# Kernel optimization log

Measured on AMD Instinct MI355X. Metric: run time of the kernel, lower is better.

## Reference

```python
import jax, jax.numpy as jnp
import numpy as np

B, C, H, W = 4, 3, 512, 960
K2 = 16  # 4x4 adaptive filter, DAIN-style


def setup_inputs() -> dict:
    key = jax.random.key(0)
    k1, k2, k3 = jax.random.split(key, 3)
    teninput = jax.random.normal(k1, (B, C, H, W), dtype=jnp.float32)
    tenflow = jax.random.normal(k2, (B, 2, H, W), dtype=jnp.float32)
    tenfilter = jax.random.uniform(k3, (B, K2, H, W), dtype=jnp.float32)
    return {"teninput": teninput, "tenflow": tenflow, "tenfilter": tenfilter}


def reference(teninput, tenflow, tenfilter):
    # DAIN FilterInterpolation forward:
    # out[b,c,y,x] = valid * sum_{dj,di < K} filter[b, dj*K+di, y, x]
    #               * bilinear(input, y2_T + dj + beta, x2_L + di + alpha)
    # with per-corner clamped gathers; out-of-bounds flow targets give 0.
    b, c, h, w = teninput.shape
    k2 = tenfilter.shape[1]
    K = int(np.sqrt(k2))

    dt = teninput.dtype
    xs = jnp.arange(w, dtype=dt)[None, None, :]
    ys = jnp.arange(h, dtype=dt)[None, :, None]
    fx, fy = tenflow[:, 0], tenflow[:, 1]          # [B,H,W]
    x2 = xs + fx
    y2 = ys + fy
    valid = ((x2 >= 0) & (x2 <= w - 1) & (y2 >= 0) & (y2 <= h - 1)
             & (jnp.abs(fx) < w / 2) & (jnp.abs(fy) < h / 2))

    ix = jnp.floor(x2).astype(jnp.int32)
    iy = jnp.floor(y2).astype(jnp.int32)
    alpha = (x2 - ix)[:, None]                     # [B,1,H,W]
    beta = (y2 - iy)[:, None]
    ixL0 = ix + 1 - K // 2                         # window left edge
    iyT0 = iy + 1 - K // 2                         # window top edge

    inp_flat = teninput.reshape(b, c, h * w)

    def gather(yi, xi):  # yi, xi: [B,H,W] int -> [B,C,H,W]
        idx = (yi * w + xi).reshape(b, 1, h * w)
        return jnp.take_along_axis(inp_flat, idx, axis=2).reshape(b, c, h, w)

    wTL = (1 - alpha) * (1 - beta)
    wTR = alpha * (1 - beta)
    wBL = (1 - alpha) * beta
    wBR = alpha * beta

    out = jnp.zeros_like(teninput)
    for dj in range(K):
        yT = jnp.clip(iyT0 + dj, 0, h - 1)
        yB = jnp.clip(iyT0 + dj + 1, 0, h - 1)
        for di in range(K):
            xL = jnp.clip(ixL0 + di, 0, w - 1)
            xR = jnp.clip(ixL0 + di + 1, 0, w - 1)
            val = (wTL * gather(yT, xL) + wTR * gather(yT, xR)
                   + wBL * gather(yB, xL) + wBR * gather(yB, xR))
            out = out + val * tenfilter[:, dj * K + di][:, None]

    return out * valid[:, None].astype(dt)
```

## Files before the change

### kernel.cpp

```cpp
#include <hip/hip_runtime.h>

#define BB 4
#define CC 3
#define HH 512
#define WW 960
#define HW (HH * WW)

typedef float f4 __attribute__((ext_vector_type(4)));

__global__ __launch_bounds__(256)
void filter_interp_batch(const float* __restrict__ inp,
                         const float* __restrict__ flow,
                         const float* __restrict__ filt,
                         float* __restrict__ out) {
    const int bpi = HW / 256;
    const int b   = blockIdx.x / bpi;
    const int rem = (blockIdx.x - b * bpi) * 256 + threadIdx.x;
    const int y   = rem / WW;
    const int x   = rem - y * WW;

    const float* flb = flow + (size_t)(b * 2) * HW;
    const float fx = flb[rem];
    const float fy = flb[rem + HW];

    float ftv[16];
    const float* fb = filt + (size_t)(b * 16) * HW + rem;
#pragma unroll
    for (int k = 0; k < 16; ++k) ftv[k] = fb[(size_t)k * HW];

    const float x2 = (float)x + fx;
    const float y2 = (float)y + fy;
    const bool valid = (x2 >= 0.0f) && (x2 <= (float)(WW - 1)) &&
                       (y2 >= 0.0f) && (y2 <= (float)(HH - 1)) &&
                       (fabsf(fx) < (float)WW * 0.5f) &&
                       (fabsf(fy) < (float)HH * 0.5f);

    const float fxf = floorf(x2);
    const float fyf = floorf(y2);
    const float alpha = valid ? (x2 - fxf) : 0.0f;
    const float beta  = valid ? (y2 - fyf) : 0.0f;
    const int   ix    = valid ? (int)fxf : 480;
    const int   iy    = valid ? (int)fyf : 256;
    const float vf    = valid ? 1.0f : 0.0f;

    const float wTL = vf * (1.0f - alpha) * (1.0f - beta);
    const float wTR = vf * alpha * (1.0f - beta);
    const float wBL = vf * (1.0f - alpha) * beta;
    const float wBR = vf * alpha * beta;

    const int ixL0 = ix - 1;
    const int iyT0 = iy - 1;
    int R[5];
#pragma unroll
    for (int j = 0; j < 5; ++j) R[j] = min(max(iyT0 + j, 0), HH - 1);

    const float* ib = inp + (size_t)(b * CC) * HW;

    f4 acc4[CC];
#pragma unroll
    for (int c = 0; c < CC; ++c) acc4[c] = (f4){0.f, 0.f, 0.f, 0.f};
    float accs[CC] = {0.f, 0.f, 0.f};

    const bool fast = (ixL0 >= 0) && (ixL0 <= WW - 5);
    if (fast) {
        const int a0 = ixL0 & ~3;
        const int o  = ixL0 - a0;

        f4 P[30];
#pragma unroll
        for (int j = 0; j < 5; ++j) {
            const int ro = R[j] * WW + a0;
#pragma unroll
            for (int c = 0; c < CC; ++c) {
                const float* p = ib + (size_t)c * HW + ro;
                P[(j * 3 + c) * 2 + 0] = *(const f4*)(p);
                P[(j * 3 + c) * 2 + 1] = *(const f4*)(p + 4);
            }
        }

        float Wm[5][5];
#pragma unroll
        for (int j = 0; j < 5; ++j)
#pragma unroll
            for (int i = 0; i < 5; ++i) Wm[j][i] = 0.0f;
#pragma unroll
        for (int dj = 0; dj < 4; ++dj) {
#pragma unroll
            for (int di = 0; di < 4; ++di) {
                const float f = ftv[dj * 4 + di];
                Wm[dj][di]         += f * wTL;
                Wm[dj][di + 1]     += f * wTR;
                Wm[dj + 1][di]     += f * wBL;
                Wm[dj + 1][di + 1] += f * wBR;
            }
        }

        const bool s2 = (o & 2) != 0;
        const bool s1 = (o & 1) != 0;
        f4 WL[5], WH[5];
#pragma unroll
        for (int j = 0; j < 5; ++j) {
            float t[8];
#pragma unroll
            for (int i = 0; i < 8; ++i) t[i] = (i < 5) ? Wm[j][i] : 0.0f;
            float u[8];
#pragma unroll
            for (int i = 0; i < 8; ++i)
                u[i] = s2 ? ((i >= 2) ? t[i - 2] : 0.0f) : t[i];
            float w[8];
#pragma unroll
            for (int i = 0; i < 8; ++i)
                w[i] = s1 ? ((i >= 1) ? u[i - 1] : 0.0f) : u[i];
            WL[j] = (f4){w[0], w[1], w[2], w[3]};
            WH[j] = (f4){w[4], w[5], w[6], w[7]};
        }

#pragma unroll
        for (int j = 0; j < 5; ++j) {
#pragma unroll
            for (int c = 0; c < CC; ++c) {
                acc4[c] += P[(j * 3 + c) * 2 + 0] * WL[j];
                acc4[c] += P[(j * 3 + c) * 2 + 1] * WH[j];
            }
        }
    } else {
        float Wm[5][5];
#pragma unroll
        for (int j = 0; j < 5; ++j)
#pragma unroll
            for (int i = 0; i < 5; ++i) Wm[j][i] = 0.0f;
#pragma unroll
        for (int dj = 0; dj < 4; ++dj) {
#pragma unroll
            for (int di = 0; di < 4; ++di) {
                const float f = ftv[dj * 4 + di];
                Wm[dj][di]         += f * wTL;
                Wm[dj][di + 1]     += f * wTR;
                Wm[dj + 1][di]     += f * wBL;
                Wm[dj + 1][di + 1] += f * wBR;
            }
        }
        int S[5];
#pragma unroll
        for (int i = 0; i < 5; ++i) S[i] = min(max(ixL0 + i, 0), WW - 1);
#pragma unroll
        for (int c = 0; c < CC; ++c) {
            const float* ic = ib + (size_t)c * HW;
            float a = 0.0f;
#pragma unroll
            for (int j = 0; j < 5; ++j) {
                const float* row = ic + (size_t)R[j] * WW;
#pragma unroll
                for (int i = 0; i < 5; ++i) a += row[S[i]] * Wm[j][i];
            }
            accs[c] = a;
        }
    }

    float* ob = out + (size_t)(b * CC) * HW + rem;
#pragma unroll
    for (int c = 0; c < CC; ++c) {
        ob[(size_t)c * HW] =
            acc4[c][0] + acc4[c][1] + acc4[c][2] + acc4[c][3] + accs[c];
    }
}

extern "C" void kernel_launch(void* const* d_in, const int* in_sizes, int n_in,
                              void* d_out, int out_size, void* d_ws, size_t ws_size,
                              hipStream_t stream) {
    const float* teninput  = (const float*)d_in[0];
    const float* tenflow   = (const float*)d_in[1];
    const float* tenfilter = (const float*)d_in[2];
    float* out = (float*)d_out;

    const int blocks = (BB * HW) / 256;
    filter_interp_batch<<<blocks, 256, 0, stream>>>(teninput, tenflow, tenfilter, out);
}
```

Baseline: 243.0 us.

## Process four rows per thread with 64x16 tiles and front-loaded flow/filter loads

Each thread now handles four vertically adjacent pixels in a 64-wide by 16-tall block tile instead of one pixel per thread. All flow and filter values for the four pixels (72 loads) are issued up front to raise memory-level parallelism. The 2D tile is meant to improve cache locality of the gathered input rows, and launch bounds now request two blocks per CU. The cost is much higher register pressure, which risks spilling or lower occupancy, and a quarter as many threads in total.

```diff
diff --git a/kernel.cpp b/kernel.cpp
--- a/kernel.cpp
+++ b/kernel.cpp
@@ -5,163 +5,182 @@
 #define HH 512
 #define WW 960
 #define HW (HH * WW)
+#define YD 4
+#define NTX (WW / 64)
+#define NTG (HH / (4 * YD))
 
 typedef float f4 __attribute__((ext_vector_type(4)));
 
-__global__ __launch_bounds__(256)
-void filter_interp_batch(const float* __restrict__ inp,
-                         const float* __restrict__ flow,
-                         const float* __restrict__ filt,
-                         float* __restrict__ out) {
-    const int bpi = HW / 256;
-    const int b   = blockIdx.x / bpi;
-    const int rem = (blockIdx.x - b * bpi) * 256 + threadIdx.x;
-    const int y   = rem / WW;
-    const int x   = rem - y * WW;
+__global__ __launch_bounds__(256, 2)
+void filter_interp_col(const float* __restrict__ inp,
+                       const float* __restrict__ flow,
+                       const float* __restrict__ filt,
+                       float* __restrict__ out) {
+    const int lx = threadIdx.x & 63;
+    const int ly = threadIdx.x >> 6;
+    int blk = blockIdx.x;
+    const int b  = blk / (NTG * NTX);
+    int r        = blk - b * (NTG * NTX);
+    const int tg = r / NTX;
+    const int tx = r - tg * NTX;
+
+    const int x  = tx * 64 + lx;
+    const int y0 = tg * (4 * YD) + ly * YD;
 
     const float* flb = flow + (size_t)(b * 2) * HW;
-    const float fx = flb[rem];
-    const float fy = flb[rem + HW];
+    const float* fb  = filt + (size_t)(b * 16) * HW;
+    const float* ib  = inp  + (size_t)(b * CC) * HW;
+    float*       ob  = out  + (size_t)(b * CC) * HW;
 
-    float ftv[16];
-    const float* fb = filt + (size_t)(b * 16) * HW + rem;
+    float fxv[YD], fyv[YD], ftv[YD][16];
 #pragma unroll
-    for (int k = 0; k < 16; ++k) ftv[k] = fb[(size_t)k * HW];
+    for (int k = 0; k < YD; ++k) {
+        const int rem = (y0 + k) * WW + x;
+        fxv[k] = flb[rem];
+        fyv[k] = flb[rem + HW];
+#pragma unroll
+        for (int t = 0; t < 16; ++t) ftv[k][t] = fb[(size_t)t * HW + rem];
+    }
 
-    const float x2 = (float)x + fx;
-    const float y2 = (float)y + fy;
-    const bool valid = (x2 >= 0.0f) && (x2 <= (float)(WW - 1)) &&
-                       (y2 >= 0.0f) && (y2 <= (float)(HH - 1)) &&
-                       (fabsf(fx) < (float)WW * 0.5f) &&
-                       (fabsf(fy) < (float)HH * 0.5f);
+#pragma unroll
+    for (int k = 0; k < YD; ++k) {
+        const int y   = y0 + k;
+        const int rem = y * WW + x;
+        const float fx = fxv[k];
+        const float fy = fyv[k];
 
-    const float fxf = floorf(x2);
-    const float fyf = floorf(y2);
-    const float alpha = valid ? (x2 - fxf) : 0.0f;
-    const float beta  = valid ? (y2 - fyf) : 0.0f;
-    const int   ix    = valid ? (int)fxf : 480;
-    const int   iy    = valid ? (int)fyf : 256;
-    const float vf    = valid ? 1.0f : 0.0f;
+        const float x2 = (float)x + fx;
+        const float y2 = (float)y + fy;
+        const bool valid = (x2 >= 0.0f) && (x2 <= (float)(WW - 1)) &&
+                           (y2 >= 0.0f) && (y2 <= (float)(HH - 1)) &&
+                           (fabsf(fx) < (float)WW * 0.5f) &&
+                           (fabsf(fy) < (float)HH * 0.5f);
 
-    const float wTL = vf * (1.0f - alpha) * (1.0f - beta);
-    const float wTR = vf * alpha * (1.0f - beta);
-    const float wBL = vf * (1.0f - alpha) * beta;
-    const float wBR = vf * alpha * beta;
+        const float fxf = floorf(x2);
+        const float fyf = floorf(y2);
+        const float alpha = valid ? (x2 - fxf) : 0.0f;
+        const float beta  = valid ? (y2 - fyf) : 0.0f;
+        const int   ix    = valid ? (int)fxf : 480;
+        const int   iy    = valid ? (int)fyf : 256;
+        const float vf    = valid ? 1.0f : 0.0f;
 
-    const int ixL0 = ix - 1;
-    const int iyT0 = iy - 1;
-    int R[5];
+        const float wTL = vf * (1.0f - alpha) * (1.0f - beta);
+        const float wTR = vf * alpha * (1.0f - beta);
+        const float wBL = vf * (1.0f - alpha) * beta;
+        const float wBR = vf * alpha * beta;
+
+        const int ixL0 = ix - 1;
+        const int iyT0 = iy - 1;
+        int R[5];
 #pragma unroll
-    for (int j = 0; j < 5; ++j) R[j] = min(max(iyT0 + j, 0), HH - 1);
+        for (int j = 0; j < 5; ++j) R[j] = min(max(iyT0 + j, 0), HH - 1);
 
-    const float* ib = inp + (size_t)(b * CC) * HW;
+        f4 acc4[CC];
+#pragma unroll
+        for (int c = 0; c < CC; ++c) acc4[c] = (f4){0.f, 0.f, 0.f, 0.f};
+        float accs[CC] = {0.f, 0.f, 0.f};
 
-    f4 acc4[CC];
+        const bool fast = (ixL0 >= 0) && (ixL0 <= WW - 5);
+        if (fast) {
+            const int a0 = ixL0 & ~3;
+            const int o  = ixL0 - a0;
+
+            f4 P[30];
 #pragma unroll
-    for (int c = 0; c < CC; ++c) acc4[c] = (f4){0.f, 0.f, 0.f, 0.f};
-    float accs[CC] = {0.f, 0.f, 0.f};
+            for (int j = 0; j < 5; ++j) {
+                const int ro = R[j] * WW + a0;
+#pragma unroll
+                for (int c = 0; c < CC; ++c) {
+                    const float* p = ib + (size_t)c * HW + ro;
+                    P[(j * 3 + c) * 2 + 0] = *(const f4*)(p);
+                    P[(j * 3 + c) * 2 + 1] = *(const f4*)(p + 4);
+                }
+            }
 
-    const bool fast = (ixL0 >= 0) && (ixL0 <= WW - 5);
-    if (fast) {
-        const int a0 = ixL0 & ~3;
-        const int o  = ixL0 - a0;
+            float Wm[5][5];
+#pragma unroll
+            for (int j = 0; j < 5; ++j)
+#pragma unroll
+                for (int i = 0; i < 5; ++i) Wm[j][i] = 0.0f;
+#pragma unroll
+            for (int dj = 0; dj < 4; ++dj) {
+#pragma unroll
+                for (int di = 0; di < 4; ++di) {
+                    const float f = ftv[k][dj * 4 + di];
+                    Wm[dj][di]         += f * wTL;
+                    Wm[dj][di + 1]     += f * wTR;
+                    Wm[dj + 1][di]     += f * wBL;
+                    Wm[dj + 1][di + 1] += f * wBR;
+                }
+            }
 
-        f4 P[30];
+            const bool s2 = (o & 2) != 0;
+            const bool s1 = (o & 1) != 0;
+            f4 WL[5], WH[5];
 #pragma unroll
-        for (int j = 0; j < 5; ++j) {
-            const int ro = R[j] * WW + a0;
+            for (int j = 0; j < 5; ++j) {
+                float t[8];
+#pragma unroll
+                for (int i = 0; i < 8; ++i) t[i] = (i < 5) ? Wm[j][i] : 0.0f;
+                float u[8];
+#pragma unroll
+                for (int i = 0; i < 8; ++i)
+                    u[i] = s2 ? ((i >= 2) ? t[i - 2] : 0.0f) : t[i];
+                float w[8];
+#pragma unroll
+                for (int i = 0; i < 8; ++i)
+                    w[i] = s1 ? ((i >= 1) ? u[i - 1] : 0.0f) : u[i];
+                WL[j] = (f4){w[0], w[1], w[2], w[3]};
+                WH[j] = (f4){w[4], w[5], w[6], w[7]};
+            }
+
+#pragma unroll
+            for (int j = 0; j < 5; ++j) {
+#pragma unroll
+                for (int c = 0; c < CC; ++c) {
+                    acc4[c] += P[(j * 3 + c) * 2 + 0] * WL[j];
+                    acc4[c] += P[(j * 3 + c) * 2 + 1] * WH[j];
+                }
+            }
+        } else {
+            float Wm[5][5];
+#pragma unroll
+            for (int j = 0; j < 5; ++j)
+#pragma unroll
+                for (int i = 0; i < 5; ++i) Wm[j][i] = 0.0f;
+#pragma unroll
+            for (int dj = 0; dj < 4; ++dj) {
+#pragma unroll
+                for (int di = 0; di < 4; ++di) {
+                    const float f = ftv[k][dj * 4 + di];
+                    Wm[dj][di]         += f * wTL;
+                    Wm[dj][di + 1]     += f * wTR;
+                    Wm[dj + 1][di]     += f * wBL;
+                    Wm[dj + 1][di + 1] += f * wBR;
+                }
+            }
+            int S[5];
+#pragma unroll
+            for (int i = 0; i < 5; ++i) S[i] = min(max(ixL0 + i, 0), WW - 1);
 #pragma unroll
             for (int c = 0; c < CC; ++c) {
-                const float* p = ib + (size_t)c * HW + ro;
-                P[(j * 3 + c) * 2 + 0] = *(const f4*)(p);
-                P[(j * 3 + c) * 2 + 1] = *(const f4*)(p + 4);
+                const float* ic = ib + (size_t)c * HW;
+                float a = 0.0f;
+#pragma unroll
+                for (int j = 0; j < 5; ++j) {
+                    const float* row = ic + (size_t)R[j] * WW;
+#pragma unroll
+                    for (int i = 0; i < 5; ++i) a += row[S[i]] * Wm[j][i];
+                }
+                accs[c] = a;
             }
         }
 
-        float Wm[5][5];
-#pragma unroll
-        for (int j = 0; j < 5; ++j)
-#pragma unroll
-            for (int i = 0; i < 5; ++i) Wm[j][i] = 0.0f;
-#pragma unroll
-        for (int dj = 0; dj < 4; ++dj) {
-#pragma unroll
-            for (int di = 0; di < 4; ++di) {
-                const float f = ftv[dj * 4 + di];
-                Wm[dj][di]         += f * wTL;
-                Wm[dj][di + 1]     += f * wTR;
-                Wm[dj + 1][di]     += f * wBL;
-                Wm[dj + 1][di + 1] += f * wBR;
-            }
-        }
-
-        const bool s2 = (o & 2) != 0;
-        const bool s1 = (o & 1) != 0;
-        f4 WL[5], WH[5];
-#pragma unroll
-        for (int j = 0; j < 5; ++j) {
-            float t[8];
-#pragma unroll
-            for (int i = 0; i < 8; ++i) t[i] = (i < 5) ? Wm[j][i] : 0.0f;
-            float u[8];
-#pragma unroll
-            for (int i = 0; i < 8; ++i)
-                u[i] = s2 ? ((i >= 2) ? t[i - 2] : 0.0f) : t[i];
-            float w[8];
-#pragma unroll
-            for (int i = 0; i < 8; ++i)
-                w[i] = s1 ? ((i >= 1) ? u[i - 1] : 0.0f) : u[i];
-            WL[j] = (f4){w[0], w[1], w[2], w[3]};
-            WH[j] = (f4){w[4], w[5], w[6], w[7]};
-        }
-
-#pragma unroll
-        for (int j = 0; j < 5; ++j) {
-#pragma unroll
-            for (int c = 0; c < CC; ++c) {
-                acc4[c] += P[(j * 3 + c) * 2 + 0] * WL[j];
-                acc4[c] += P[(j * 3 + c) * 2 + 1] * WH[j];
-            }
-        }
-    } else {
-        float Wm[5][5];
-#pragma unroll
-        for (int j = 0; j < 5; ++j)
-#pragma unroll
-            for (int i = 0; i < 5; ++i) Wm[j][i] = 0.0f;
-#pragma unroll
-        for (int dj = 0; dj < 4; ++dj) {
-#pragma unroll
-            for (int di = 0; di < 4; ++di) {
-                const float f = ftv[dj * 4 + di];
-                Wm[dj][di]         += f * wTL;
-                Wm[dj][di + 1]     += f * wTR;
-                Wm[dj + 1][di]     += f * wBL;
-                Wm[dj + 1][di + 1] += f * wBR;
-            }
-        }
-        int S[5];
-#pragma unroll
-        for (int i = 0; i < 5; ++i) S[i] = min(max(ixL0 + i, 0), WW - 1);
 #pragma unroll
         for (int c = 0; c < CC; ++c) {
-            const float* ic = ib + (size_t)c * HW;
-            float a = 0.0f;
-#pragma unroll
-            for (int j = 0; j < 5; ++j) {
-                const float* row = ic + (size_t)R[j] * WW;
-#pragma unroll
-                for (int i = 0; i < 5; ++i) a += row[S[i]] * Wm[j][i];
-            }
-            accs[c] = a;
+            ob[(size_t)c * HW + rem] =
+                acc4[c][0] + acc4[c][1] + acc4[c][2] + acc4[c][3] + accs[c];
         }
-    }
-
-    float* ob = out + (size_t)(b * CC) * HW + rem;
-#pragma unroll
-    for (int c = 0; c < CC; ++c) {
-        ob[(size_t)c * HW] =
-            acc4[c][0] + acc4[c][1] + acc4[c][2] + acc4[c][3] + accs[c];
     }
 }
 
@@ -173,6 +192,6 @@
     const float* tenfilter = (const float*)d_in[2];
     float* out = (float*)d_out;
 
-    const int blocks = (BB * HW) / 256;
-    filter_interp_batch<<<blocks, 256, 0, stream>>>(teninput, tenflow, tenfilter, out);
+    const int blocks = BB * NTG * NTX;
+    filter_interp_col<<<blocks, 256, 0, stream>>>(teninput, tenflow, tenfilter, out);
 }
```

Measured after the change: 250.9 us. 1.03x slower.
